# Kernel tuning notes

Hardware: AMD Instinct MI355X
Metric: run time of the kernel (lower is better)

## Reference

```python
import jax, jax.numpy as jnp
import numpy as np

B, L, V, D = 512, 41, 4, 64        # batch, seq_len=41 (hard-coded in source), vocab=DNA, d_model=64
NL, DI, N, DTR, K = 3, 128, 16, 4, 4  # n_layer, d_inner=2*D, d_state, dt_rank=ceil(D/16), d_conv
NS = 3  # three parallel stacks (layers1/2/3)


def setup_inputs() -> dict:
    key = jax.random.key(0)
    ks = jax.random.split(key, 16)
    s = 0.02
    nrm = lambda k, sh: jax.random.normal(k, sh, jnp.float32) * s
    A_log = jnp.log(jnp.arange(1, N + 1, dtype=jnp.float32))  # S4D-real init
    return {
        "input_ids": jax.random.randint(ks[0], (B, L), 0, V),
        "embedding": nrm(ks[1], (V, D)),
        # per-stack, per-layer Mamba block params, stacked [NS, NL, ...]
        "in_proj": nrm(ks[2], (NS, NL, D, 2 * DI)),
        "conv_w": nrm(ks[3], (NS, NL, DI, 1, K)),
        "conv_b": jnp.zeros((NS, NL, DI), jnp.float32),
        "x_proj": nrm(ks[4], (NS, NL, DI, DTR + 2 * N)),
        "dt_w": nrm(ks[5], (NS, NL, DTR, DI)),
        "dt_b": jnp.full((NS, NL, DI), -2.0, jnp.float32),
        "A_log": jnp.broadcast_to(A_log, (NS, NL, DI, N)) + 0.0,
        "Dp": jnp.ones((NS, NL, DI), jnp.float32),
        "out_proj": nrm(ks[6], (NS, NL, DI, D)),
        "norm_w": jnp.ones((NS, NL, D), jnp.float32),
        "norm_f_w": jnp.ones((D,), jnp.float32),
        "fusion_w": jnp.zeros((NS,), jnp.float32),  # softmax-weighted fusion of the 3 representations
        # LastDense MLP head: 64*41 -> 384 -> 16 -> 1 (dropout is eval-mode identity)
        "W1": nrm(ks[7], (D * L, 384)), "b1": jnp.zeros((384,), jnp.float32),
        "W2": nrm(ks[8], (384, 16)), "b2": jnp.zeros((16,), jnp.float32),
        "W3": nrm(ks[9], (16, 1)), "b3": jnp.zeros((1,), jnp.float32),
    }


def rmsnorm(x, w, eps=1e-5):
    return x * jax.lax.rsqrt(jnp.mean(x * x, axis=-1, keepdims=True) + eps) * w


def silu(x):
    return x * jax.nn.sigmoid(x)


def mamba_block(x, ip, cw, cb, xp, dw, db, al, dp, op):
    # x: [B, L, D]
    bsz = x.shape[0]
    u, res = jnp.split(x @ ip, 2, axis=-1)  # each [B, L, DI]
    # causal depthwise conv1d (torch padding=3 then [..., :L] == left-pad K-1)
    uc = jax.lax.conv_general_dilated(
        u.transpose(0, 2, 1), cw, window_strides=(1,), padding=[(K - 1, 0)],
        feature_group_count=DI, dimension_numbers=("NCH", "OIH", "NCH"))
    u = silu((uc + cb[None, :, None]).transpose(0, 2, 1))  # [B, L, DI]
    dbl = u @ xp  # [B, L, DTR+2N]
    dt = jax.nn.softplus(dbl[..., :DTR] @ dw + db)           # [B, L, DI]
    Bm = dbl[..., DTR:DTR + N]                               # [B, L, N]
    C = dbl[..., DTR + N:]                                   # [B, L, N]
    A = -jnp.exp(al)                                         # [DI, N]
    dA = jnp.exp(dt[..., None] * A)                          # [B, L, DI, N]
    dBu = dt[..., None] * Bm[:, :, None, :] * u[..., None]   # [B, L, DI, N]

    def step(h, xs):
        dA_t, dBu_t, C_t = xs
        h = dA_t * h + dBu_t                                 # [B, DI, N]
        return h, jnp.einsum("bdn,bn->bd", h, C_t)

    h0 = jnp.zeros((bsz, DI, N), x.dtype)
    _, ys = jax.lax.scan(step, h0, (dA.transpose(1, 0, 2, 3), dBu.transpose(1, 0, 2, 3), C.transpose(1, 0, 2)))
    y = ys.transpose(1, 0, 2) + u * dp                       # [B, L, DI]
    return (y * silu(res)) @ op                              # [B, L, D]


def _forward(input_ids, embedding, in_proj, conv_w, conv_b, x_proj, dt_w, dt_b,
             A_log, Dp, out_proj, norm_w, norm_f_w, fusion_w, W1, b1, W2, b2, W3, b3):
    emb = embedding[input_ids]  # [B, L, D]

    def run_stack(ip, cw, cb, xp, dw, db, al, dp, op, nw):
        x = emb
        for i in range(NL):  # residual: x + MambaBlock(RMSNorm(x))
            x = x + mamba_block(rmsnorm(x, nw[i]), ip[i], cw[i], cb[i], xp[i], dw[i], db[i], al[i], dp[i], op[i])
        return x

    stack_out = jax.vmap(run_stack)(in_proj, conv_w, conv_b, x_proj, dt_w, dt_b,
                                    A_log, Dp, out_proj, norm_w)  # [NS, B, L, D]
    stack_out = rmsnorm(stack_out, norm_f_w)  # final norm_f per stack
    fused = jnp.einsum("s,sbld->bld", jax.nn.softmax(fusion_w), stack_out)  # fusion of 3 reps
    flat = fused.reshape(fused.shape[0], L * D)
    h = jax.nn.relu(flat @ W1 + b1)
    h = jax.nn.relu(h @ W2 + b2)
    logits = (h @ W3 + b3)[:, 0]
    return jax.nn.sigmoid(logits)  # [B]


def reference(input_ids, embedding, in_proj, conv_w, conv_b, x_proj, dt_w, dt_b,
              A_log, Dp, out_proj, norm_w, norm_f_w, fusion_w, W1, b1, W2, b2, W3, b3):
    return _forward(input_ids, embedding, in_proj, conv_w, conv_b, x_proj, dt_w, dt_b,
                    A_log, Dp, out_proj, norm_w, norm_f_w, fusion_w, W1, b1, W2, b2, W3, b3)
```

## Files before the change

kernel.cpp:

```cpp
#include <hip/hip_runtime.h>
#include <hip/hip_bf16.h>
#include <math.h>

#define Bq  512
#define Lq  41
#define Vq  4
#define Dq  64
#define NLq 3
#define DIq 128
#define Nq  16
#define DTRq 4
#define Kq  4
#define NSq 3
#define H1q 384
#define H2q 16
#define FLATq (Lq*Dq)

typedef __attribute__((ext_vector_type(8))) short frag8;
typedef __attribute__((ext_vector_type(4))) float f32x4;

__device__ __forceinline__ float b2f(unsigned short u) {
    union { float f; unsigned int i; } v; v.i = ((unsigned int)u) << 16; return v.f;
}
__device__ __forceinline__ unsigned short f2b_rne(float f) {
    union { float f; unsigned int i; } v; v.f = f;
    unsigned int x = v.i;
    return (unsigned short)((x + 0x7fffu + ((x >> 16) & 1u)) >> 16);
}
__device__ __forceinline__ unsigned short f2b_tr(float f) {
    union { float f; unsigned int i; } v; v.f = f;
    return (unsigned short)(v.i >> 16);
}
__device__ __forceinline__ float fast_rcp(float x) { return __builtin_amdgcn_rcpf(x); }

__global__ __launch_bounds__(256) void prep_kernel(const float* __restrict__ W1,
                                                   const float* __restrict__ in_proj,
                                                   const float* __restrict__ x_proj,
                                                   const float* __restrict__ out_proj,
                                                   const float* __restrict__ A_log,
                                                   unsigned short* __restrict__ W1b,
                                                   unsigned short* __restrict__ Wb_in,
                                                   unsigned short* __restrict__ xp_b,
                                                   unsigned short* __restrict__ op_b,
                                                   int* __restrict__ Aflag) {
    const int bx = blockIdx.x;
    if (bx < 246) {
        __shared__ float t[64][65];
        const int k0 = (bx / 6) * 64, n0 = (bx % 6) * 64;
        for (int idx = threadIdx.x; idx < 4096; idx += 256) {
            int kr = idx >> 6, nc = idx & 63;
            t[kr][nc] = W1[(size_t)(k0 + kr) * H1q + n0 + nc];
        }
        __syncthreads();
        for (int idx = threadIdx.x; idx < 4096; idx += 256) {
            int nr = idx >> 6, kc = idx & 63;
            W1b[(size_t)(n0 + nr) * FLATq + k0 + kc] = f2b_rne(t[kc][nr]);
        }
        return;
    }
    if (bx == 246 + 1080) {
        const int tid = threadIdx.x;
        const int d = tid >> 1, half = tid & 1;
        for (int sl = 0; sl < 9; ++sl) {
            const float* al = A_log + (size_t)sl * (DIq * Nq) + d * Nq + half * 8;
            float A2[8];
            #pragma unroll
            for (int n = 0; n < 8; ++n) A2[n] = -__expf(al[n]);
            float d0 = A2[1] - A2[0];
            int ok = 1;
            #pragma unroll
            for (int n = 2; n < 8; ++n) {
                float dk = A2[n] - A2[n-1];
                if (!(fabsf(dk - d0) <= 1e-4f * fabsf(d0) + 1e-12f)) ok = 0;
            }
            int allok = __syncthreads_and(ok);
            if (tid == 0) Aflag[sl] = allok;
        }
        return;
    }
    int idx = (bx - 246) * 256 + threadIdx.x;
    if (idx < 9*256*64) {
        int sl = idx >> 14, rem = idx & 16383;
        int n = rem >> 6, k = rem & 63;
        Wb_in[idx] = f2b_rne(in_proj[(size_t)sl*16384 + k*256 + n]);
    } else if (idx < 9*256*64 + 9*48*128) {
        int i2 = idx - 9*256*64;
        int sl = i2 / 6144, rem = i2 % 6144;
        int c = rem >> 7, k = rem & 127;
        float v = (c < 36) ? x_proj[(size_t)sl*(128*36) + k*36 + c] : 0.f;
        xp_b[i2] = f2b_rne(v);
    } else if (idx < 9*256*64 + 9*48*128 + 9*64*128) {
        int i3 = idx - (9*256*64 + 9*48*128);
        int sl = i3 >> 13, rem = i3 & 8191;
        int n = rem >> 7, k = rem & 127;
        op_b[i3] = f2b_rne(out_proj[(size_t)sl*8192 + k*64 + n]);
    }
}

__global__ __launch_bounds__(256, 2) void mamba_stack(
    unsigned short* __restrict__ Xn,
    const int* __restrict__ ids,
    const float* __restrict__ emb,
    const unsigned short* __restrict__ Wb_in,
    const float* __restrict__ conv_w,
    const float* __restrict__ conv_b,
    const unsigned short* __restrict__ xp_b,
    const float* __restrict__ dt_w,
    const float* __restrict__ dt_b,
    const float* __restrict__ A_log,
    const float* __restrict__ Dp,
    const unsigned short* __restrict__ op_b,
    const float* __restrict__ norm_w,
    const float* __restrict__ norm_f_w,
    const float* __restrict__ fusion_w,
    const int* __restrict__ Aflag)
{
    const int b = blockIdx.x, s = blockIdx.y, tid = threadIdx.x;
    const int wave = tid >> 6, lane = tid & 63;
    const int nl = lane & 15, quad = lane >> 4;

    __shared__ float          xt  [Lq][76];
    __shared__ unsigned short u_lb[Lq][136];
    __shared__ unsigned short rs_lb[Lq][132];
    __shared__ __align__(16) char un_buf[6560];
    unsigned short (*xn_lb)[72] = (unsigned short(*)[72])un_buf;
    float          (*dbl_s)[40] = (float(*)[40])un_buf;

    for (int l = wave; l < Lq; l += 4) {
        int id = ids[b * Lq + l];
        xt[l][lane] = emb[id * Dq + lane];
    }

    for (int layer = 0; layer < NLq; ++layer) {
        const int sl = s * NLq + layer;

        {
            const float nwv = norm_w[(size_t)sl * Dq + lane];
            for (int l = wave; l < Lq; l += 4) {
                float v  = xt[l][lane];
                float ss = v * v;
                #pragma unroll
                for (int off = 32; off; off >>= 1) ss += __shfl_xor(ss, off, 64);
                float scale = __builtin_amdgcn_rsqf(ss * (1.0f / Dq) + 1e-5f);
                xn_lb[l][lane] = f2b_tr(v * scale * nwv);
            }
        }
        __syncthreads();

        {
            #pragma unroll
            for (int t = 0; t < 12; ++t) {
                const int id = wave * 12 + t;
                const int mt = id >> 4, nt = id & 15;
                int ar = mt * 16 + nl; if (ar > Lq - 1) ar = Lq - 1;
                const unsigned short* Wp = Wb_in + ((size_t)(sl * 256 + nt * 16 + nl)) * 64 + quad * 8;
                frag8 a0 = *(const frag8*)&xn_lb[ar][quad * 8];
                frag8 a1 = *(const frag8*)&xn_lb[ar][32 + quad * 8];
                frag8 b0 = *(const frag8*)&Wp[0];
                frag8 b1 = *(const frag8*)&Wp[32];
                f32x4 c = {0.f, 0.f, 0.f, 0.f};
                c = __builtin_amdgcn_mfma_f32_16x16x32_bf16(a0, b0, c, 0, 0, 0);
                c = __builtin_amdgcn_mfma_f32_16x16x32_bf16(a1, b1, c, 0, 0, 0);
                const int col = nt * 16 + nl;
                const int r0 = mt * 16 + quad * 4;
                if (col < DIq) {
                    #pragma unroll
                    for (int r = 0; r < 4; ++r) {
                        int row = r0 + r;
                        if (row < Lq) u_lb[row][col] = f2b_tr(c[r]);
                    }
                } else {
                    const int d = col - DIq;
                    #pragma unroll
                    for (int r = 0; r < 4; ++r) {
                        int row = r0 + r;
                        if (row < Lq) {
                            float v = c[r];
                            rs_lb[row][d] = f2b_tr(v * fast_rcp(1.f + __expf(-v)));
                        }
                    }
                }
            }
        }
        __syncthreads();

        {
            const float* cw = conv_w + (size_t)sl * (DIq * Kq);
            const int d = tid >> 1, half = tid & 1;
            const float c0 = cw[d*4+0], c1 = cw[d*4+1], c2 = cw[d*4+2], c3 = cw[d*4+3];
            const float cbv = conv_b[(size_t)sl * DIq + d];
            float w0 = 0.f, w1 = 0.f, w2 = 0.f;
            if (half) { w0 = b2f(u_lb[18][d]); w1 = b2f(u_lb[19][d]); w2 = b2f(u_lb[20][d]); }
            const int base = half ? 21 : 0;
            const int cnt  = half ? 20 : 21;
            for (int i = 0; i < cnt; ++i) {
                int l = base + i;
                float cur = b2f(u_lb[l][d]);
                float a = fmaf(w0, c0, fmaf(w1, c1, fmaf(w2, c2, fmaf(cur, c3, cbv))));
                u_lb[l][d] = f2b_tr(a * fast_rcp(1.f + __expf(-a)));
                w0 = w1; w1 = w2; w2 = cur;
            }
        }
        __syncthreads();

        {
            for (int t = wave; t < 9; t += 4) {
                const int mt = t / 3, ct = t % 3;
                int ar = mt * 16 + nl; if (ar > Lq - 1) ar = Lq - 1;
                f32x4 c = {0.f, 0.f, 0.f, 0.f};
                #pragma unroll
                for (int kt = 0; kt < 4; ++kt) {
                    frag8 a  = *(const frag8*)&u_lb[ar][kt * 32 + quad * 8];
                    frag8 bb = *(const frag8*)&xp_b[((size_t)(sl * 48 + ct * 16 + nl)) * 128 + kt * 32 + quad * 8];
                    c = __builtin_amdgcn_mfma_f32_16x16x32_bf16(a, bb, c, 0, 0, 0);
                }
                const int col = ct * 16 + nl, r0 = mt * 16 + quad * 4;
                if (col < 40) {
                    #pragma unroll
                    for (int r = 0; r < 4; ++r) {
                        int row = r0 + r;
                        if (row < Lq) dbl_s[row][col] = c[r];
                    }
                }
            }
        }
        __syncthreads();

        {
            const int d = tid >> 1, half = tid & 1;
            const float* al = A_log + (size_t)sl * (DIq * Nq) + d * Nq + half * 8;
            float A2[8], h[8];
            #pragma unroll
            for (int n = 0; n < 8; ++n) {
                A2[n] = -__expf(al[n]) * 1.442695041f;
                h[n] = 0.f;
            }
            const float dd = A2[1] - A2[0];
            const bool fastA = __builtin_amdgcn_readfirstlane(Aflag[sl]) != 0;
            const float* dw = dt_w + (size_t)sl * (DTRq * DIq);
            const float dw0 = dw[d], dw1 = dw[DIq + d], dw2 = dw[2*DIq + d], dw3 = dw[3*DIq + d];
            const float dbv = dt_b[(size_t)sl * DIq + d];
            const float dpd = Dp[(size_t)sl * DIq + d];

            auto step = [&](int l, float dt_) {
                float u_  = b2f(u_lb[l][d]);
                float4 B0 = *(const float4*)&dbl_s[l][4  + half * 8];
                float4 B1 = *(const float4*)&dbl_s[l][8  + half * 8];
                float4 C0 = *(const float4*)&dbl_s[l][20 + half * 8];
                float4 C1 = *(const float4*)&dbl_s[l][24 + half * 8];
                float dtu = dt_ * u_;
                float a0, a1, a2, a3, a4, a5, a6, a7;
                if (fastA) {
                    a0 = __builtin_amdgcn_exp2f(dt_ * A2[0]);
                    float r = __builtin_amdgcn_exp2f(dt_ * dd);
                    a1 = a0 * r; a2 = a1 * r; a3 = a2 * r; a4 = a3 * r;
                    a5 = a4 * r; a6 = a5 * r; a7 = a6 * r;
                } else {
                    a0 = __builtin_amdgcn_exp2f(dt_ * A2[0]);
                    a1 = __builtin_amdgcn_exp2f(dt_ * A2[1]);
                    a2 = __builtin_amdgcn_exp2f(dt_ * A2[2]);
                    a3 = __builtin_amdgcn_exp2f(dt_ * A2[3]);
                    a4 = __builtin_amdgcn_exp2f(dt_ * A2[4]);
                    a5 = __builtin_amdgcn_exp2f(dt_ * A2[5]);
                    a6 = __builtin_amdgcn_exp2f(dt_ * A2[6]);
                    a7 = __builtin_amdgcn_exp2f(dt_ * A2[7]);
                }
                float y = 0.f;
                h[0] = fmaf(a0, h[0], B0.x * dtu); y = fmaf(h[0], C0.x, y);
                h[1] = fmaf(a1, h[1], B0.y * dtu); y = fmaf(h[1], C0.y, y);
                h[2] = fmaf(a2, h[2], B0.z * dtu); y = fmaf(h[2], C0.z, y);
                h[3] = fmaf(a3, h[3], B0.w * dtu); y = fmaf(h[3], C0.w, y);
                h[4] = fmaf(a4, h[4], B1.x * dtu); y = fmaf(h[4], C1.x, y);
                h[5] = fmaf(a5, h[5], B1.y * dtu); y = fmaf(h[5], C1.y, y);
                h[6] = fmaf(a6, h[6], B1.z * dtu); y = fmaf(h[6], C1.z, y);
                h[7] = fmaf(a7, h[7], B1.w * dtu); y = fmaf(h[7], C1.w, y);
                y += __shfl_xor(y, 1, 64);
                if (!half) {
                    float rsv = b2f(rs_lb[l][d]);
                    u_lb[l][d] = f2b_tr(fmaf(u_, dpd, y) * rsv);
                }
            };

            for (int l0 = 0; l0 < Lq; l0 += 2) {
                int lme = l0 + half; if (lme > Lq - 1) lme = Lq - 1;
                float4 q0 = *(const float4*)&dbl_s[lme][0];
                float x = fmaf(q0.x, dw0, fmaf(q0.y, dw1, fmaf(q0.z, dw2, fmaf(q0.w, dw3, dbv))));
                float dts = fmaxf(x, 0.f) + __logf(1.f + __expf(-fabsf(x)));
                float dto = __shfl_xor(dts, 1, 64);
                step(l0, half ? dto : dts);
                if (l0 + 1 < Lq) step(l0 + 1, half ? dts : dto);
            }
        }
        __syncthreads();

        {
            const int ntG = wave;
            for (int mt = 0; mt < 3; ++mt) {
                int ar = mt * 16 + nl; if (ar > Lq - 1) ar = Lq - 1;
                f32x4 c = {0.f, 0.f, 0.f, 0.f};
                #pragma unroll
                for (int kt = 0; kt < 4; ++kt) {
                    frag8 a  = *(const frag8*)&u_lb[ar][kt * 32 + quad * 8];
                    frag8 bb = *(const frag8*)&op_b[((size_t)(sl * 64 + ntG * 16 + nl)) * 128 + kt * 32 + quad * 8];
                    c = __builtin_amdgcn_mfma_f32_16x16x32_bf16(a, bb, c, 0, 0, 0);
                }
                const int j = ntG * 16 + nl, r0 = mt * 16 + quad * 4;
                #pragma unroll
                for (int r = 0; r < 4; ++r) {
                    int row = r0 + r;
                    if (row < Lq) xt[row][j] += c[r];
                }
            }
        }
        __syncthreads();
    }

    {
        float fw0 = fusion_w[0], fw1 = fusion_w[1], fw2 = fusion_w[2];
        float mx = fmaxf(fw0, fmaxf(fw1, fw2));
        float e0 = __expf(fw0 - mx), e1 = __expf(fw1 - mx), e2 = __expf(fw2 - mx);
        float sw = (s == 0 ? e0 : (s == 1 ? e1 : e2)) * fast_rcp(e0 + e1 + e2);
        float nf = norm_f_w[lane] * sw;
        unsigned short* xr = Xn + ((size_t)s * Bq + b) * FLATq;
        for (int l = wave; l < Lq; l += 4) {
            float v  = xt[l][lane];
            float ss = v * v;
            #pragma unroll
            for (int off = 32; off; off >>= 1) ss += __shfl_xor(ss, off, 64);
            float scale = __builtin_amdgcn_rsqf(ss * (1.0f / Dq) + 1e-5f);
            xr[l * Dq + lane] = f2b_tr(v * scale * nf);
        }
    }
}

__global__ __launch_bounds__(256) void head_gemm1(const unsigned short* __restrict__ Xn,
                                                  const unsigned short* __restrict__ W1b,
                                                  const float* __restrict__ b1,
                                                  float* __restrict__ H1) {
    const int tid = threadIdx.x;
    const int wave = tid >> 6, lane = tid & 63;
    const int nl = lane & 15, quad = lane >> 4;
    const int mt = blockIdx.x, nt = blockIdx.y;

    __shared__ float red[4][16][17];

    const int kbeg = (wave < 2) ? wave * 21 : 42 + (wave - 2) * 20;
    const int kcnt = (wave < 2) ? 21 : 20;
    const size_t SB = (size_t)Bq * FLATq;
    const unsigned short* A0 = Xn  + (size_t)(mt * 16 + nl) * FLATq + quad * 8;
    const unsigned short* Br = W1b + (size_t)(nt * 16 + nl) * FLATq + quad * 8;

    f32x4 c = {0.f, 0.f, 0.f, 0.f};
    for (int ks = kbeg; ks < kbeg + kcnt; ++ks) {
        const int off = ks * 32;
        frag8 bb = *(const frag8*)(Br + off);
        frag8 a0 = *(const frag8*)(A0 + off);
        frag8 a1 = *(const frag8*)(A0 + SB + off);
        frag8 a2 = *(const frag8*)(A0 + 2 * SB + off);
        c = __builtin_amdgcn_mfma_f32_16x16x32_bf16(a0, bb, c, 0, 0, 0);
        c = __builtin_amdgcn_mfma_f32_16x16x32_bf16(a1, bb, c, 0, 0, 0);
        c = __builtin_amdgcn_mfma_f32_16x16x32_bf16(a2, bb, c, 0, 0, 0);
    }
    #pragma unroll
    for (int r = 0; r < 4; ++r) red[wave][quad * 4 + r][nl] = c[r];
    __syncthreads();

    const int row = tid >> 4, colv = tid & 15;
    float acc = red[0][row][colv] + red[1][row][colv]
              + red[2][row][colv] + red[3][row][colv];
    const int col = nt * 16 + colv;
    H1[(size_t)(mt * 16 + row) * H1q + col] = fmaxf(acc + b1[col], 0.f);
}

__global__ __launch_bounds__(256) void head_final(const float* __restrict__ H1,
                                                  const float* __restrict__ W2,
                                                  const float* __restrict__ b2,
                                                  const float* __restrict__ W3,
                                                  const float* __restrict__ b3,
                                                  float* __restrict__ out) {
    const int b0 = blockIdx.x * 16, tid = threadIdx.x;
    __shared__ float H1s[16 * H1q];
    __shared__ float h2s[16][16];
    for (int idx = tid; idx < 16 * H1q; idx += 256)
        H1s[idx] = H1[(size_t)b0 * H1q + idx];
    __syncthreads();
    {
        const int row = tid >> 4, g = tid & 15;
        float acc = b2[g];
        for (int k = 0; k < H1q; ++k)
            acc = fmaf(H1s[row * H1q + k], W2[k * H2q + g], acc);
        h2s[row][g] = fmaxf(acc, 0.f);
    }
    __syncthreads();
    if (tid < 16) {
        float z = b3[0];
        #pragma unroll
        for (int k = 0; k < H2q; ++k) z = fmaf(h2s[tid][k], W3[k], z);
        out[b0 + tid] = fast_rcp(1.f + __expf(-z));
    }
}

extern "C" void kernel_launch(void* const* d_in, const int* in_sizes, int n_in,
                              void* d_out, int out_size, void* d_ws, size_t ws_size,
                              hipStream_t stream) {
    const int*   ids      = (const int*)  d_in[0];
    const float* emb      = (const float*)d_in[1];
    const float* in_proj  = (const float*)d_in[2];
    const float* conv_w   = (const float*)d_in[3];
    const float* conv_b   = (const float*)d_in[4];
    const float* x_proj   = (const float*)d_in[5];
    const float* dt_w     = (const float*)d_in[6];
    const float* dt_b     = (const float*)d_in[7];
    const float* A_log    = (const float*)d_in[8];
    const float* Dp       = (const float*)d_in[9];
    const float* out_proj = (const float*)d_in[10];
    const float* norm_w   = (const float*)d_in[11];
    const float* norm_f_w = (const float*)d_in[12];
    const float* fusion_w = (const float*)d_in[13];
    const float* W1       = (const float*)d_in[14];
    const float* b1       = (const float*)d_in[15];
    const float* W2       = (const float*)d_in[16];
    const float* b2       = (const float*)d_in[17];
    const float* W3       = (const float*)d_in[18];
    const float* b3       = (const float*)d_in[19];
    float* out = (float*)d_out;

    unsigned short* Xn    = (unsigned short*)d_ws;
    unsigned short* Wb_in = Xn    + (size_t)NSq * Bq * FLATq;
    unsigned short* xp_b  = Wb_in + 9*256*64;
    unsigned short* op_b  = xp_b  + 9*48*128;
    unsigned short* W1b   = op_b  + 9*64*128;
    float*          H1    = (float*)(W1b + (size_t)H1q * FLATq);
    int*            Aflag = (int*)H1;

    hipLaunchKernelGGL(prep_kernel, dim3(246 + 1080 + 1), dim3(256), 0, stream,
                       W1, in_proj, x_proj, out_proj, A_log, W1b, Wb_in, xp_b, op_b, Aflag);

    hipLaunchKernelGGL(mamba_stack, dim3(Bq, NSq), dim3(256), 0, stream,
                       Xn, ids, emb, Wb_in, conv_w, conv_b, xp_b, dt_w, dt_b,
                       A_log, Dp, op_b, norm_w, norm_f_w, fusion_w, Aflag);

    hipLaunchKernelGGL(head_gemm1, dim3(Bq/16, H1q/64), dim3(256), 0, stream,
                       Xn, W1b, b1, H1);

    hipLaunchKernelGGL(head_final, dim3(Bq/16), dim3(256), 0, stream,
                       H1, W2, b2, W3, b3, out);
}
```

Before: 296.6 us.

## Double mamba_stack block to 512 threads, splitting scan state across four lanes

Launches the per-sample Mamba stack kernel with 512 threads instead of 256 and redistributes every phase across eight waves. The selective scan now gives each channel four lanes holding four states each, reducing y with two xor shuffles, and the causal conv splits the sequence into four segments. The aim is to shorten the serial per-thread scan chain and raise parallelism per block, at the cost of more shuffles, more idle waves in the small GEMM phases, and possibly lower occupancy per CU.

```diff
diff --git a/kernel.cpp b/kernel.cpp
--- a/kernel.cpp
+++ b/kernel.cpp
@@ -97,7 +97,7 @@
     }
 }
 
-__global__ __launch_bounds__(256, 2) void mamba_stack(
+__global__ __launch_bounds__(512, 2) void mamba_stack(
     unsigned short* __restrict__ Xn,
     const int* __restrict__ ids,
     const float* __restrict__ emb,
@@ -126,7 +126,7 @@
     unsigned short (*xn_lb)[72] = (unsigned short(*)[72])un_buf;
     float          (*dbl_s)[40] = (float(*)[40])un_buf;
 
-    for (int l = wave; l < Lq; l += 4) {
+    for (int l = wave; l < Lq; l += 8) {
         int id = ids[b * Lq + l];
         xt[l][lane] = emb[id * Dq + lane];
     }
@@ -136,7 +136,7 @@
 
         {
             const float nwv = norm_w[(size_t)sl * Dq + lane];
-            for (int l = wave; l < Lq; l += 4) {
+            for (int l = wave; l < Lq; l += 8) {
                 float v  = xt[l][lane];
                 float ss = v * v;
                 #pragma unroll
@@ -149,8 +149,8 @@
 
         {
             #pragma unroll
-            for (int t = 0; t < 12; ++t) {
-                const int id = wave * 12 + t;
+            for (int t = 0; t < 6; ++t) {
+                const int id = wave * 6 + t;
                 const int mt = id >> 4, nt = id & 15;
                 int ar = mt * 16 + nl; if (ar > Lq - 1) ar = Lq - 1;
                 const unsigned short* Wp = Wb_in + ((size_t)(sl * 256 + nt * 16 + nl)) * 64 + quad * 8;
@@ -186,13 +186,15 @@
 
         {
             const float* cw = conv_w + (size_t)sl * (DIq * Kq);
-            const int d = tid >> 1, half = tid & 1;
+            const int d = tid >> 2, seg = tid & 3;
             const float c0 = cw[d*4+0], c1 = cw[d*4+1], c2 = cw[d*4+2], c3 = cw[d*4+3];
             const float cbv = conv_b[(size_t)sl * DIq + d];
+            const int base = (seg == 0) ? 0 : 11 + 10 * (seg - 1);
+            const int cnt  = (seg == 0) ? 11 : 10;
             float w0 = 0.f, w1 = 0.f, w2 = 0.f;
-            if (half) { w0 = b2f(u_lb[18][d]); w1 = b2f(u_lb[19][d]); w2 = b2f(u_lb[20][d]); }
-            const int base = half ? 21 : 0;
-            const int cnt  = half ? 20 : 21;
+            if (seg) {
+                w0 = b2f(u_lb[base-3][d]); w1 = b2f(u_lb[base-2][d]); w2 = b2f(u_lb[base-1][d]);
+            }
             for (int i = 0; i < cnt; ++i) {
                 int l = base + i;
                 float cur = b2f(u_lb[l][d]);
@@ -204,7 +206,7 @@
         __syncthreads();
 
         {
-            for (int t = wave; t < 9; t += 4) {
+            for (int t = wave; t < 9; t += 8) {
                 const int mt = t / 3, ct = t % 3;
                 int ar = mt * 16 + nl; if (ar > Lq - 1) ar = Lq - 1;
                 f32x4 c = {0.f, 0.f, 0.f, 0.f};
@@ -227,11 +229,11 @@
         __syncthreads();
 
         {
-            const int d = tid >> 1, half = tid & 1;
-            const float* al = A_log + (size_t)sl * (DIq * Nq) + d * Nq + half * 8;
-            float A2[8], h[8];
+            const int d = tid >> 2, q4 = tid & 3;
+            const float* al = A_log + (size_t)sl * (DIq * Nq) + d * Nq + q4 * 4;
+            float A2[4], h[4];
             #pragma unroll
-            for (int n = 0; n < 8; ++n) {
+            for (int n = 0; n < 4; ++n) {
                 A2[n] = -__expf(al[n]) * 1.442695041f;
                 h[n] = 0.f;
             }
@@ -241,61 +243,55 @@
             const float dw0 = dw[d], dw1 = dw[DIq + d], dw2 = dw[2*DIq + d], dw3 = dw[3*DIq + d];
             const float dbv = dt_b[(size_t)sl * DIq + d];
             const float dpd = Dp[(size_t)sl * DIq + d];
+            const int lbase = lane & 60;
 
             auto step = [&](int l, float dt_) {
                 float u_  = b2f(u_lb[l][d]);
-                float4 B0 = *(const float4*)&dbl_s[l][4  + half * 8];
-                float4 B1 = *(const float4*)&dbl_s[l][8  + half * 8];
-                float4 C0 = *(const float4*)&dbl_s[l][20 + half * 8];
-                float4 C1 = *(const float4*)&dbl_s[l][24 + half * 8];
+                float4 Bv = *(const float4*)&dbl_s[l][4  + q4 * 4];
+                float4 Cv = *(const float4*)&dbl_s[l][20 + q4 * 4];
                 float dtu = dt_ * u_;
-                float a0, a1, a2, a3, a4, a5, a6, a7;
+                float a0, a1, a2, a3;
                 if (fastA) {
                     a0 = __builtin_amdgcn_exp2f(dt_ * A2[0]);
                     float r = __builtin_amdgcn_exp2f(dt_ * dd);
-                    a1 = a0 * r; a2 = a1 * r; a3 = a2 * r; a4 = a3 * r;
-                    a5 = a4 * r; a6 = a5 * r; a7 = a6 * r;
+                    a1 = a0 * r; a2 = a1 * r; a3 = a2 * r;
                 } else {
                     a0 = __builtin_amdgcn_exp2f(dt_ * A2[0]);
                     a1 = __builtin_amdgcn_exp2f(dt_ * A2[1]);
                     a2 = __builtin_amdgcn_exp2f(dt_ * A2[2]);
                     a3 = __builtin_amdgcn_exp2f(dt_ * A2[3]);
-                    a4 = __builtin_amdgcn_exp2f(dt_ * A2[4]);
-                    a5 = __builtin_amdgcn_exp2f(dt_ * A2[5]);
-                    a6 = __builtin_amdgcn_exp2f(dt_ * A2[6]);
-                    a7 = __builtin_amdgcn_exp2f(dt_ * A2[7]);
                 }
                 float y = 0.f;
-                h[0] = fmaf(a0, h[0], B0.x * dtu); y = fmaf(h[0], C0.x, y);
-                h[1] = fmaf(a1, h[1], B0.y * dtu); y = fmaf(h[1], C0.y, y);
-                h[2] = fmaf(a2, h[2], B0.z * dtu); y = fmaf(h[2], C0.z, y);
-                h[3] = fmaf(a3, h[3], B0.w * dtu); y = fmaf(h[3], C0.w, y);
-                h[4] = fmaf(a4, h[4], B1.x * dtu); y = fmaf(h[4], C1.x, y);
-                h[5] = fmaf(a5, h[5], B1.y * dtu); y = fmaf(h[5], C1.y, y);
-                h[6] = fmaf(a6, h[6], B1.z * dtu); y = fmaf(h[6], C1.z, y);
-                h[7] = fmaf(a7, h[7], B1.w * dtu); y = fmaf(h[7], C1.w, y);
+                h[0] = fmaf(a0, h[0], Bv.x * dtu); y = fmaf(h[0], Cv.x, y);
+                h[1] = fmaf(a1, h[1], Bv.y * dtu); y = fmaf(h[1], Cv.y, y);
+                h[2] = fmaf(a2, h[2], Bv.z * dtu); y = fmaf(h[2], Cv.z, y);
+                h[3] = fmaf(a3, h[3], Bv.w * dtu); y = fmaf(h[3], Cv.w, y);
                 y += __shfl_xor(y, 1, 64);
-                if (!half) {
+                y += __shfl_xor(y, 2, 64);
+                if (q4 == 0) {
                     float rsv = b2f(rs_lb[l][d]);
                     u_lb[l][d] = f2b_tr(fmaf(u_, dpd, y) * rsv);
                 }
             };
 
-            for (int l0 = 0; l0 < Lq; l0 += 2) {
-                int lme = l0 + half; if (lme > Lq - 1) lme = Lq - 1;
-                float4 q0 = *(const float4*)&dbl_s[lme][0];
-                float x = fmaf(q0.x, dw0, fmaf(q0.y, dw1, fmaf(q0.z, dw2, fmaf(q0.w, dw3, dbv))));
+            for (int l0 = 0; l0 < Lq; l0 += 4) {
+                int lme = l0 + q4; if (lme > Lq - 1) lme = Lq - 1;
+                float4 qv = *(const float4*)&dbl_s[lme][0];
+                float x = fmaf(qv.x, dw0, fmaf(qv.y, dw1, fmaf(qv.z, dw2, fmaf(qv.w, dw3, dbv))));
                 float dts = fmaxf(x, 0.f) + __logf(1.f + __expf(-fabsf(x)));
-                float dto = __shfl_xor(dts, 1, 64);
-                step(l0, half ? dto : dts);
-                if (l0 + 1 < Lq) step(l0 + 1, half ? dts : dto);
-            }
-        }
-        __syncthreads();
-
-        {
-            const int ntG = wave;
-            for (int mt = 0; mt < 3; ++mt) {
+                #pragma unroll
+                for (int j = 0; j < 4; ++j) {
+                    if (l0 + j >= Lq) break;
+                    float dt_ = __shfl(dts, lbase | j, 64);
+                    step(l0 + j, dt_);
+                }
+            }
+        }
+        __syncthreads();
+
+        {
+            for (int t = wave; t < 12; t += 8) {
+                const int mt = t >> 2, ntG = t & 3;
                 int ar = mt * 16 + nl; if (ar > Lq - 1) ar = Lq - 1;
                 f32x4 c = {0.f, 0.f, 0.f, 0.f};
                 #pragma unroll
@@ -322,7 +318,7 @@
         float sw = (s == 0 ? e0 : (s == 1 ? e1 : e2)) * fast_rcp(e0 + e1 + e2);
         float nf = norm_f_w[lane] * sw;
         unsigned short* xr = Xn + ((size_t)s * Bq + b) * FLATq;
-        for (int l = wave; l < Lq; l += 4) {
+        for (int l = wave; l < Lq; l += 8) {
             float v  = xt[l][lane];
             float ss = v * v;
             #pragma unroll
@@ -436,7 +432,7 @@
     hipLaunchKernelGGL(prep_kernel, dim3(246 + 1080 + 1), dim3(256), 0, stream,
                        W1, in_proj, x_proj, out_proj, A_log, W1b, Wb_in, xp_b, op_b, Aflag);
 
-    hipLaunchKernelGGL(mamba_stack, dim3(Bq, NSq), dim3(256), 0, stream,
+    hipLaunchKernelGGL(mamba_stack, dim3(Bq, NSq), dim3(512), 0, stream,
                        Xn, ids, emb, Wb_in, conv_w, conv_b, xp_b, dt_w, dt_b,
                        A_log, Dp, op_b, norm_w, norm_f_w, fusion_w, Aflag);
 
```

After: 328.3 us. 1.11x slower.
